# Kernel optimization log

Hardware: AMD Instinct MI355X
Metric: run time of the kernel (lower is better)

Reference implementation:

```python
import jax, jax.numpy as jnp
import numpy as np

N = 50000      # nodes
E = 800000     # edges (avg degree 16)
NE = 100000    # query edges
IN = 128; HID = 128; OUT = 128; FEAT = 2


def _linear_params(k, fan_in, fan_out):
    # torch.nn.Linear default init: U(-1/sqrt(fan_in), 1/sqrt(fan_in))
    s = 1.0 / np.sqrt(fan_in)
    k1, k2 = jax.random.split(k)
    W = jax.random.uniform(k1, (fan_in, fan_out), jnp.float32, -s, s)
    b = jax.random.uniform(k2, (fan_out,), jnp.float32, -s, s)
    return W, b


def setup_inputs() -> dict:
    key = jax.random.key(0)
    ks = jax.random.split(key, 9)
    inp = {}
    inp["x"] = jax.random.normal(ks[0], (N, IN), jnp.float32)
    inp["adj_t"] = jax.random.randint(ks[1], (2, E), 0, N)          # edge_index [2,E]
    inp["train_edges"] = jax.random.randint(ks[2], (NE, 2), 0, N)   # query edges
    # GCNConv stack params (lin weight + bias per layer)
    inp["W1"], inp["b1"] = _linear_params(ks[3], IN, HID)
    inp["W2"], inp["b2"] = _linear_params(ks[4], HID, HID)
    inp["W3"], inp["b3"] = _linear_params(ks[5], HID, OUT)
    # LinkPredictor MLP params
    inp["P1"], inp["pb1"] = _linear_params(ks[6], OUT, HID)
    inp["P2"], inp["pb2"] = _linear_params(ks[7], HID, HID)
    inp["P3"], inp["pb3"] = _linear_params(ks[8], HID, FEAT)
    return inp


def gcn_conv(x, edge_index, W, b):
    # GCNConv(normalize=False), edge_weight=None:
    #   h = x @ W; out[dst] += h[src]; out += bias
    h = x @ W                                    # [N, d_out]
    msg = h[edge_index[0]]                       # gather  [E, d_out]
    out = jax.ops.segment_sum(msg, edge_index[1], num_segments=x.shape[0])
    return out + b


def reference(x, adj_t, train_edges, W1, b1, W2, b2, W3, b3, P1, pb1, P2, pb2, P3, pb3):
    # GCN trunk (eval mode -> dropout is identity; dropout=0 anyway)
    h = jax.nn.relu(gcn_conv(x, adj_t, W1, b1))
    h = jax.nn.relu(gcn_conv(h, adj_t, W2, b2))
    emb = gcn_conv(h, adj_t, W3, b3)             # [N, OUT]
    # LinkPredictor on (src, dst) node-embedding pairs
    z = emb[train_edges[:, 0]] * emb[train_edges[:, 1]]   # [NE, OUT]
    z = jax.nn.relu(z @ P1 + pb1)
    z = jax.nn.relu(z @ P2 + pb2)
    z = z @ P3 + pb3                                       # [NE, FEAT]
    # F.normalize(p=2, dim=-1) with eps=1e-12
    z = z / jnp.maximum(jnp.linalg.norm(z, axis=-1, keepdims=True), 1e-12)
    pred = jax.nn.log_softmax(z, axis=-1)
    return pred[None]                                      # torch.unsqueeze(pred, 0)
```

## Files before the change

### kernel.cpp

```cpp
#include <hip/hip_runtime.h>
#include <math.h>

#define N_NODES 50000
#define N_EDGES 800000
#define N_QE    100000
#define D       128
#define NB      391
#define PCHUNK  8192

typedef _Float16 half8 __attribute__((ext_vector_type(8)));
typedef short    short8 __attribute__((ext_vector_type(8)));
typedef float    f32x4 __attribute__((ext_vector_type(4)));

static __device__ inline short f2bf(float f) {
    unsigned u = __builtin_bit_cast(unsigned, f);
    u += 0x7FFFu + ((u >> 16) & 1u);
    return (short)(u >> 16);
}

static const size_t O_CNT = 0;
static const size_t O_OFF = 256u * 1024;
static const size_t O_BC  = 512u * 1024;
static const size_t O_BS  = 768u * 1024;
static const size_t O_SRC = 1024u * 1024;
static const size_t O_TMP = 4u << 20;
static const size_t O_G   = 8u << 20;
static const size_t O_H   = O_G + 12800000u;
static const size_t O_T   = O_H + 12800000u;

__global__ void k_count(const int* __restrict__ dst, int* __restrict__ cnt) {
    int e = blockIdx.x * 256 + threadIdx.x;
    if (e < N_EDGES) atomicAdd(&cnt[dst[e]], 1);
}

__global__ __launch_bounds__(256)
void k_scan1(const int* __restrict__ cnt, int* __restrict__ off,
             int* __restrict__ bsum) {
    __shared__ int sh[256];
    const int t = threadIdx.x;
    const int i = blockIdx.x * 256 + t;
    int v = (i < N_NODES) ? cnt[i] : 0;
    sh[t] = v;
    __syncthreads();
    #pragma unroll
    for (int o = 1; o < 256; o <<= 1) {
        int u = (t >= o) ? sh[t - o] : 0;
        __syncthreads();
        sh[t] += u;
        __syncthreads();
    }
    if (i < N_NODES) off[i] = sh[t] - v;
    if (t == 255) bsum[blockIdx.x] = sh[255];
}

__global__ __launch_bounds__(256)
void k_scan2(int* __restrict__ bsum, int nblk) {
    __shared__ int sh[256];
    const int t = threadIdx.x;
    int v = (t < nblk) ? bsum[t] : 0;
    sh[t] = v;
    __syncthreads();
    #pragma unroll
    for (int o = 1; o < 256; o <<= 1) {
        int u = (t >= o) ? sh[t - o] : 0;
        __syncthreads();
        sh[t] += u;
        __syncthreads();
    }
    if (t < nblk) bsum[t] = sh[t] - v;
}

__global__ __launch_bounds__(256)
void k_scan3(int* __restrict__ off, const int* __restrict__ bsum) {
    const int i = blockIdx.x * 256 + threadIdx.x;
    if (i < N_NODES) off[i] = off[i] + bsum[blockIdx.x];
    if (i == 0) off[N_NODES] = N_EDGES;
}

__global__ void k_binit(const int* __restrict__ off, int* __restrict__ bcur) {
    int b = blockIdx.x * 256 + threadIdx.x;
    if (b < NB) bcur[b] = off[b << 7];
}

__global__ __launch_bounds__(256)
void k_part(const int* __restrict__ src, const int* __restrict__ dst,
            int* __restrict__ bcur, unsigned* __restrict__ tmp)
{
    __shared__ int hcnt[NB];
    __shared__ int lpos[NB];
    __shared__ int base[NB];
    const int t = threadIdx.x;
    const int e0 = blockIdx.x * PCHUNK;
    const int e1 = (e0 + PCHUNK < N_EDGES) ? e0 + PCHUNK : N_EDGES;

    for (int b = t; b < NB; b += 256) { hcnt[b] = 0; lpos[b] = 0; }
    __syncthreads();
    for (int e = e0 + t; e < e1; e += 256)
        atomicAdd(&hcnt[dst[e] >> 7], 1);
    __syncthreads();
    for (int b = t; b < NB; b += 256) {
        int c = hcnt[b];
        base[b] = c ? atomicAdd(&bcur[b], c) : 0;
    }
    __syncthreads();
    for (int e = e0 + t; e < e1; e += 256) {
        int d = dst[e];
        int b = d >> 7;
        int pos = atomicAdd(&lpos[b], 1);
        tmp[base[b] + pos] = (unsigned)src[e] | ((unsigned)(d & 127) << 16);
    }
}

__global__ __launch_bounds__(256)
void k_fine(const unsigned* __restrict__ tmp, const int* __restrict__ off,
            unsigned short* __restrict__ srcs)
{
    __shared__ int fcur[129];
    const int t = threadIdx.x;
    const int b = blockIdx.x;
    const int n0 = b << 7;
    const int nn = (N_NODES - n0 < 128) ? N_NODES - n0 : 128;
    if (t <= nn) fcur[t] = off[n0 + t];
    const int r0 = off[n0];
    const int r1 = off[n0 + nn];
    __syncthreads();
    for (int i = r0 + t; i < r1; i += 256) {
        unsigned en = tmp[i];
        int dl = en >> 16;
        int p = atomicAdd(&fcur[dl], 1);
        srcs[p] = (unsigned short)(en & 0xFFFFu);
    }
}

__global__ __launch_bounds__(256)
void k_t16all(const float* __restrict__ W1, const float* __restrict__ W2,
              const float* __restrict__ W3, const float* __restrict__ Q1,
              const float* __restrict__ Q2, short* __restrict__ T)
{
    int m = blockIdx.x >> 6;
    const float* S = (m == 0) ? W1 : (m == 1) ? W2 : (m == 2) ? W3
                   : (m == 3) ? Q1 : Q2;
    short* Dp = T + m * 16384;
    int idx = (blockIdx.x & 63) * 256 + threadIdx.x;
    int c = idx & 127, k = idx >> 7;
    Dp[c * 128 + k] = f2bf(S[k * 128 + c]);
}


template<typename XT>
__global__ __launch_bounds__(256)
void k_mm(const XT* __restrict__ X, const short* __restrict__ WT,
          _Float16* __restrict__ Y, int rows)
{
    __shared__ __align__(16) short xs[64 * 128];
    const int tid = threadIdx.x;
    const int l   = tid & 63;
    const int w   = tid >> 6;
    const int g   = l >> 4;
    const int l15 = l & 15;
    const int row0 = blockIdx.x * 64;

    {
        int r = tid >> 2;
        int gr = row0 + r; if (gr >= rows) gr = rows - 1;
        const XT* src = X + (size_t)gr * D;
        #pragma unroll
        for (int it = 0; it < 4; ++it) {
            int s = (tid & 3) + it * 4;
            short8 h;
            if constexpr (sizeof(XT) == 4) {
                float4 v0 = *(const float4*)((const float*)src + s * 8);
                float4 v1 = *(const float4*)((const float*)src + s * 8 + 4);
                h[0] = f2bf(v0.x); h[1] = f2bf(v0.y);
                h[2] = f2bf(v0.z); h[3] = f2bf(v0.w);
                h[4] = f2bf(v1.x); h[5] = f2bf(v1.y);
                h[6] = f2bf(v1.z); h[7] = f2bf(v1.w);
            } else {
                half8 v = *(const half8*)((const _Float16*)src + s * 8);
                #pragma unroll
                for (int c = 0; c < 8; ++c) h[c] = f2bf((float)v[c]);
            }
            *(short8*)&xs[r * 128 + ((s ^ (r & 7)) * 8)] = h;
        }
    }

    short8 wf[2][4];
    #pragma unroll
    for (int tt = 0; tt < 2; ++tt) {
        int c = w * 32 + tt * 16 + l15;
        #pragma unroll
        for (int s = 0; s < 4; ++s)
            wf[tt][s] = *(const short8*)(WT + (size_t)c * 128 + s * 32 + g * 8);
    }

    __syncthreads();

    f32x4 acc[4][2];
    #pragma unroll
    for (int rt = 0; rt < 4; ++rt)
        #pragma unroll
        for (int tt = 0; tt < 2; ++tt)
            acc[rt][tt] = (f32x4){0.f, 0.f, 0.f, 0.f};

    #pragma unroll
    for (int rt = 0; rt < 4; ++rt) {
        const int r = rt * 16 + l15;
        short8 a[4];
        #pragma unroll
        for (int s = 0; s < 4; ++s) {
            int slot = (4 * s + g) ^ (r & 7);
            a[s] = *(const short8*)&xs[r * 128 + slot * 8];
        }
        #pragma unroll
        for (int tt = 0; tt < 2; ++tt)
            #pragma unroll
            for (int s = 0; s < 4; ++s)
                acc[rt][tt] = __builtin_amdgcn_mfma_f32_16x16x32_bf16(
                    a[s], wf[tt][s], acc[rt][tt], 0, 0, 0);
    }

    __syncthreads();

    #pragma unroll
    for (int rt = 0; rt < 4; ++rt)
        #pragma unroll
        for (int tt = 0; tt < 2; ++tt) {
            int c = w * 32 + tt * 16 + l15;
            #pragma unroll
            for (int i = 0; i < 4; ++i) {
                int row = rt * 16 + g * 4 + i;
                int slot = (c >> 3) ^ (row & 7);
                xs[row * 128 + slot * 8 + (c & 7)] =
                    (short)__builtin_bit_cast(unsigned short, (_Float16)acc[rt][tt][i]);
            }
        }
    __syncthreads();

    {
        int r = tid >> 2;
        int gr = row0 + r;
        if (gr < rows) {
            short* dstp = (short*)(Y + (size_t)gr * D);
            #pragma unroll
            for (int it = 0; it < 4; ++it) {
                int s = (tid & 3) + it * 4;
                *(short8*)(dstp + s * 8) =
                    *(const short8*)&xs[r * 128 + ((s ^ (r & 7)) * 8)];
            }
        }
    }
}

template<bool RELU>
__global__ __launch_bounds__(256)
void k_agg(const _Float16* __restrict__ Hin, const int* __restrict__ off,
           const unsigned short* __restrict__ srcs, const float* __restrict__ bias,
           _Float16* __restrict__ Hout)
{
    const int lane = threadIdx.x & 63;
    const int es   = lane >> 4;
    const int q    = lane & 15;
    const int wv   = threadIdx.x >> 6;
    const int n    = blockIdx.x * 4 + wv;
    const int j0 = __builtin_amdgcn_readfirstlane(off[n]);
    const int j1 = __builtin_amdgcn_readfirstlane(off[n + 1]);

    float acc[8] = {};
    int j = j0;

    for (; j + 16 <= j1; j += 16) {
        half8 v[4];
        #pragma unroll
        for (int k = 0; k < 4; ++k) {
            int s = srcs[j + 4 * k + es];
            v[k] = *(const half8*)(Hin + (size_t)s * D + q * 8);
        }
        #pragma unroll
        for (int k = 0; k < 4; ++k)
            #pragma unroll
            for (int c = 0; c < 8; ++c) acc[c] += (float)v[k][c];
    }
    for (; j + 4 <= j1; j += 4) {
        int s = srcs[j + es];
        half8 v = *(const half8*)(Hin + (size_t)s * D + q * 8);
        #pragma unroll
        for (int c = 0; c < 8; ++c) acc[c] += (float)v[c];
    }
    {
        int rem = j1 - j;
        if (rem > 0) {
            int s = srcs[j + (es < rem ? es : rem - 1)];
            half8 v = *(const half8*)(Hin + (size_t)s * D + q * 8);
            if (es < rem) {
                #pragma unroll
                for (int c = 0; c < 8; ++c) acc[c] += (float)v[c];
            }
        }
    }

    #pragma unroll
    for (int c = 0; c < 8; ++c) {
        acc[c] += __shfl_xor(acc[c], 16, 64);
        acc[c] += __shfl_xor(acc[c], 32, 64);
    }

    if (es == 0) {
        half8 o;
        #pragma unroll
        for (int c = 0; c < 8; ++c) {
            float t = acc[c] + bias[q * 8 + c];
            if (RELU) t = fmaxf(t, 0.f);
            o[c] = (_Float16)t;
        }
        *(half8*)(Hout + (size_t)n * D + q * 8) = o;
    }
}

__global__ __launch_bounds__(256)
void k_predm(const _Float16* __restrict__ emb, const int* __restrict__ te,
             const short* __restrict__ P1T, const float* __restrict__ pb1,
             const short* __restrict__ P2T, const float* __restrict__ pb2,
             const float* __restrict__ P3, const float* __restrict__ pb3,
             float* __restrict__ out)
{
    __shared__ __align__(16) short xs[64 * 128];
    __shared__ float red[64][8];
    const int tid = threadIdx.x;
    const int l   = tid & 63;
    const int w   = tid >> 6;
    const int g   = l >> 4;
    const int l15 = l & 15;
    const int row0 = blockIdx.x * 64;

    {
        int r = tid >> 2;
        int e = row0 + r; if (e >= N_QE) e = N_QE - 1;
        const int2 ee = *(const int2*)(te + 2 * e);
        const _Float16* sp = emb + (size_t)ee.x * D;
        const _Float16* dp = emb + (size_t)ee.y * D;
        #pragma unroll
        for (int it = 0; it < 4; ++it) {
            int s = (tid & 3) + it * 4;
            half8 a = *(const half8*)(sp + s * 8);
            half8 b = *(const half8*)(dp + s * 8);
            short8 h;
            #pragma unroll
            for (int c = 0; c < 8; ++c) h[c] = f2bf((float)a[c] * (float)b[c]);
            *(short8*)&xs[r * 128 + ((s ^ (r & 7)) * 8)] = h;
        }
    }
    __syncthreads();

    f32x4 acc[4][2];

    {
        short8 wf[2][4];
        #pragma unroll
        for (int tt = 0; tt < 2; ++tt) {
            int c = w * 32 + tt * 16 + l15;
            #pragma unroll
            for (int s = 0; s < 4; ++s)
                wf[tt][s] = *(const short8*)(P1T + (size_t)c * 128 + s * 32 + g * 8);
        }
        #pragma unroll
        for (int rt = 0; rt < 4; ++rt)
            #pragma unroll
            for (int tt = 0; tt < 2; ++tt)
                acc[rt][tt] = (f32x4){0.f, 0.f, 0.f, 0.f};

        #pragma unroll
        for (int rt = 0; rt < 4; ++rt) {
            const int r = rt * 16 + l15;
            short8 a[4];
            #pragma unroll
            for (int s = 0; s < 4; ++s) {
                int slot = (4 * s + g) ^ (r & 7);
                a[s] = *(const short8*)&xs[r * 128 + slot * 8];
            }
            #pragma unroll
            for (int tt = 0; tt < 2; ++tt)
                #pragma unroll
                for (int s = 0; s < 4; ++s)
                    acc[rt][tt] = __builtin_amdgcn_mfma_f32_16x16x32_bf16(
                        a[s], wf[tt][s], acc[rt][tt], 0, 0, 0);
        }

        float bv[2];
        #pragma unroll
        for (int tt = 0; tt < 2; ++tt) bv[tt] = pb1[w * 32 + tt * 16 + l15];

        __syncthreads();

        #pragma unroll
        for (int rt = 0; rt < 4; ++rt)
            #pragma unroll
            for (int tt = 0; tt < 2; ++tt) {
                int c = w * 32 + tt * 16 + l15;
                #pragma unroll
                for (int i = 0; i < 4; ++i) {
                    float v = fmaxf(acc[rt][tt][i] + bv[tt], 0.f);
                    int row = rt * 16 + g * 4 + i;
                    int slot = (c >> 3) ^ (row & 7);
                    xs[row * 128 + slot * 8 + (c & 7)] = f2bf(v);
                }
            }
        __syncthreads();
    }

    {
        short8 wf[2][4];
        #pragma unroll
        for (int tt = 0; tt < 2; ++tt) {
            int c = w * 32 + tt * 16 + l15;
            #pragma unroll
            for (int s = 0; s < 4; ++s)
                wf[tt][s] = *(const short8*)(P2T + (size_t)c * 128 + s * 32 + g * 8);
        }
        #pragma unroll
        for (int rt = 0; rt < 4; ++rt)
            #pragma unroll
            for (int tt = 0; tt < 2; ++tt)
                acc[rt][tt] = (f32x4){0.f, 0.f, 0.f, 0.f};

        #pragma unroll
        for (int rt = 0; rt < 4; ++rt) {
            const int r = rt * 16 + l15;
            short8 a[4];
            #pragma unroll
            for (int s = 0; s < 4; ++s) {
                int slot = (4 * s + g) ^ (r & 7);
                a[s] = *(const short8*)&xs[r * 128 + slot * 8];
            }
            #pragma unroll
            for (int tt = 0; tt < 2; ++tt)
                #pragma unroll
                for (int s = 0; s < 4; ++s)
                    acc[rt][tt] = __builtin_amdgcn_mfma_f32_16x16x32_bf16(
                        a[s], wf[tt][s], acc[rt][tt], 0, 0, 0);
        }
    }

    {
        float bv[2];
        float2 p3v[2];
        #pragma unroll
        for (int tt = 0; tt < 2; ++tt) {
            int c = w * 32 + tt * 16 + l15;
            bv[tt] = pb2[c];
            p3v[tt] = *(const float2*)(P3 + c * 2);
        }
        #pragma unroll
        for (int rt = 0; rt < 4; ++rt)
            #pragma unroll
            for (int i = 0; i < 4; ++i) {
                float z0 = fmaxf(acc[rt][0][i] + bv[0], 0.f);
                float z1 = fmaxf(acc[rt][1][i] + bv[1], 0.f);
                float p0 = z0 * p3v[0].x + z1 * p3v[1].x;
                float p1 = z0 * p3v[0].y + z1 * p3v[1].y;
                #pragma unroll
                for (int o = 1; o < 16; o <<= 1) {
                    p0 += __shfl_xor(p0, o, 64);
                    p1 += __shfl_xor(p1, o, 64);
                }
                if (l15 == 0) {
                    int row = rt * 16 + g * 4 + i;
                    red[row][w * 2]     = p0;
                    red[row][w * 2 + 1] = p1;
                }
            }
    }
    __syncthreads();

    if (tid < 64) {
        int gr = row0 + tid;
        if (gr < N_QE) {
            float p0 = red[tid][0] + red[tid][2] + red[tid][4] + red[tid][6] + pb3[0];
            float p1 = red[tid][1] + red[tid][3] + red[tid][5] + red[tid][7] + pb3[1];
            float nrm = fmaxf(sqrtf(p0 * p0 + p1 * p1), 1e-12f);
            p0 /= nrm; p1 /= nrm;
            float m = fmaxf(p0, p1);
            float lse = m + logf(expf(p0 - m) + expf(p1 - m));
            out[gr * 2]     = p0 - lse;
            out[gr * 2 + 1] = p1 - lse;
        }
    }
}

extern "C" void kernel_launch(void* const* d_in, const int* in_sizes, int n_in,
                              void* d_out, int out_size, void* d_ws, size_t ws_size,
                              hipStream_t stream)
{
    (void)in_sizes; (void)n_in; (void)out_size; (void)ws_size;
    const float* x   = (const float*)d_in[0];
    const int*   adj = (const int*)d_in[1];
    const int*   te  = (const int*)d_in[2];
    const float* W1  = (const float*)d_in[3];
    const float* b1  = (const float*)d_in[4];
    const float* W2  = (const float*)d_in[5];
    const float* b2  = (const float*)d_in[6];
    const float* W3  = (const float*)d_in[7];
    const float* b3  = (const float*)d_in[8];
    const float* P1  = (const float*)d_in[9];
    const float* pb1 = (const float*)d_in[10];
    const float* P2  = (const float*)d_in[11];
    const float* pb2 = (const float*)d_in[12];
    const float* P3  = (const float*)d_in[13];
    const float* pb3 = (const float*)d_in[14];
    float* out = (float*)d_out;

    char* ws = (char*)d_ws;
    int* cnt  = (int*)(ws + O_CNT);
    int* off  = (int*)(ws + O_OFF);
    int* bcur = (int*)(ws + O_BC);
    int* bsum = (int*)(ws + O_BS);
    unsigned short* srcs = (unsigned short*)(ws + O_SRC);
    unsigned* tmp = (unsigned*)(ws + O_TMP);
    _Float16* G = (_Float16*)(ws + O_G);
    _Float16* H = (_Float16*)(ws + O_H);
    short*    T = (short*)(ws + O_T);

    const int* esrc = adj;
    const int* edst = adj + N_EDGES;

    const int SBLK = (N_NODES + 255) / 256;

    k_t16all<<<320, 256, 0, stream>>>(W1, W2, W3, P1, P2, T);

    hipMemsetAsync(cnt, 0, N_NODES * sizeof(int), stream);
    k_count<<<N_EDGES / 256, 256, 0, stream>>>(edst, cnt);
    k_scan1<<<SBLK, 256, 0, stream>>>(cnt, off, bsum);
    k_scan2<<<1, 256, 0, stream>>>(bsum, SBLK);
    k_scan3<<<SBLK, 256, 0, stream>>>(off, bsum);
    k_binit<<<2, 256, 0, stream>>>(off, bcur);
    k_part<<<(N_EDGES + PCHUNK - 1) / PCHUNK, 256, 0, stream>>>(esrc, edst, bcur, tmp);
    k_fine<<<NB, 256, 0, stream>>>(tmp, off, srcs);

    const int gN = (N_NODES + 63) / 64;

    k_mm<float><<<gN, 256, 0, stream>>>(x, T, H, N_NODES);
    k_agg<true><<<N_NODES / 4, 256, 0, stream>>>(H, off, srcs, b1, G);
    k_mm<_Float16><<<gN, 256, 0, stream>>>(G, T + 16384, H, N_NODES);
    k_agg<true><<<N_NODES / 4, 256, 0, stream>>>(H, off, srcs, b2, G);
    k_mm<_Float16><<<gN, 256, 0, stream>>>(G, T + 2 * 16384, H, N_NODES);
    k_agg<false><<<N_NODES / 4, 256, 0, stream>>>(H, off, srcs, b3, G);

    const int gQ = (N_QE + 63) / 64;
    k_predm<<<gQ, 256, 0, stream>>>(G, te, T + 3 * 16384, pb1,
                                    T + 4 * 16384, pb2, P3, pb3, out);
}
```

Measured before the change: 331.1 us.

## Split GCN aggregation into column quarters with 8 edges per wavefront step

The aggregation kernel now splits the 128 feature columns into four 32-column slices, each handled by its own grid partition. Within a slice, each wavefront processes 4 nodes, with 8 lanes per edge loading 4 halves each, so 8 edges are read in parallel. The idea is to keep a smaller working set of H columns hot in cache per pass and to use nontemporal stores for the output. In exchange, the neighbour index lists are re-read four times, loads narrow to 8 bytes, and the loop has no unrolling, which may reduce memory-level parallelism.

```diff
diff --git a/kernel.cpp b/kernel.cpp
--- a/kernel.cpp
+++ b/kernel.cpp
@@ -7,7 +7,9 @@
 #define D       128
 #define NB      391
 #define PCHUNK  8192
-
+#define NBLKQ   3125
+
+typedef _Float16 half4q __attribute__((ext_vector_type(4)));
 typedef _Float16 half8 __attribute__((ext_vector_type(8)));
 typedef short    short8 __attribute__((ext_vector_type(8)));
 typedef float    f32x4 __attribute__((ext_vector_type(4)));
@@ -257,62 +259,51 @@
            const unsigned short* __restrict__ srcs, const float* __restrict__ bias,
            _Float16* __restrict__ Hout)
 {
-    const int lane = threadIdx.x & 63;
-    const int es   = lane >> 4;
-    const int q    = lane & 15;
-    const int wv   = threadIdx.x >> 6;
-    const int n    = blockIdx.x * 4 + wv;
-    const int j0 = __builtin_amdgcn_readfirstlane(off[n]);
-    const int j1 = __builtin_amdgcn_readfirstlane(off[n + 1]);
-
-    float acc[8] = {};
-    int j = j0;
-
-    for (; j + 16 <= j1; j += 16) {
-        half8 v[4];
-        #pragma unroll
-        for (int k = 0; k < 4; ++k) {
-            int s = srcs[j + 4 * k + es];
-            v[k] = *(const half8*)(Hin + (size_t)s * D + q * 8);
-        }
-        #pragma unroll
-        for (int k = 0; k < 4; ++k)
-            #pragma unroll
-            for (int c = 0; c < 8; ++c) acc[c] += (float)v[k][c];
-    }
-    for (; j + 4 <= j1; j += 4) {
-        int s = srcs[j + es];
-        half8 v = *(const half8*)(Hin + (size_t)s * D + q * 8);
-        #pragma unroll
-        for (int c = 0; c < 8; ++c) acc[c] += (float)v[c];
-    }
-    {
-        int rem = j1 - j;
-        if (rem > 0) {
-            int s = srcs[j + (es < rem ? es : rem - 1)];
-            half8 v = *(const half8*)(Hin + (size_t)s * D + q * 8);
-            if (es < rem) {
-                #pragma unroll
-                for (int c = 0; c < 8; ++c) acc[c] += (float)v[c];
-            }
-        }
-    }
-
-    #pragma unroll
-    for (int c = 0; c < 8; ++c) {
-        acc[c] += __shfl_xor(acc[c], 16, 64);
-        acc[c] += __shfl_xor(acc[c], 32, 64);
-    }
-
-    if (es == 0) {
-        half8 o;
-        #pragma unroll
-        for (int c = 0; c < 8; ++c) {
-            float t = acc[c] + bias[q * 8 + c];
-            if (RELU) t = fmaxf(t, 0.f);
-            o[c] = (_Float16)t;
-        }
-        *(half8*)(Hout + (size_t)n * D + q * 8) = o;
+    const int l   = threadIdx.x & 63;
+    const int wv  = threadIdx.x >> 6;
+    const int es  = l >> 3;
+    const int qq  = l & 7;
+    const int p   = blockIdx.x / NBLKQ;
+    const int nb  = blockIdx.x % NBLKQ;
+    const int colbase = p * 32 + qq * 4;
+    const float4 bb = *(const float4*)(bias + colbase);
+
+    #pragma unroll
+    for (int i = 0; i < 4; ++i) {
+        const int n = nb * 16 + wv * 4 + i;
+        const int j0 = __builtin_amdgcn_readfirstlane(off[n]);
+        const int j1 = __builtin_amdgcn_readfirstlane(off[n + 1]);
+
+        float a0 = 0.f, a1 = 0.f, a2 = 0.f, a3 = 0.f;
+        for (int j = j0; j < j1; j += 8) {
+            if (es < j1 - j) {
+                int s = srcs[j + es];
+                half4q v = *(const half4q*)(Hin + (size_t)s * D + colbase);
+                a0 += (float)v[0]; a1 += (float)v[1];
+                a2 += (float)v[2]; a3 += (float)v[3];
+            }
+        }
+        #pragma unroll
+        for (int m = 8; m < 64; m <<= 1) {
+            a0 += __shfl_xor(a0, m, 64);
+            a1 += __shfl_xor(a1, m, 64);
+            a2 += __shfl_xor(a2, m, 64);
+            a3 += __shfl_xor(a3, m, 64);
+        }
+        if (es == 0) {
+            float t0 = a0 + bb.x, t1 = a1 + bb.y;
+            float t2 = a2 + bb.z, t3 = a3 + bb.w;
+            if (RELU) {
+                t0 = fmaxf(t0, 0.f); t1 = fmaxf(t1, 0.f);
+                t2 = fmaxf(t2, 0.f); t3 = fmaxf(t3, 0.f);
+            }
+            half4q o;
+            o[0] = (_Float16)t0; o[1] = (_Float16)t1;
+            o[2] = (_Float16)t2; o[3] = (_Float16)t3;
+            __builtin_nontemporal_store(
+                __builtin_bit_cast(unsigned long long, o),
+                (unsigned long long*)(Hout + (size_t)n * D + colbase));
+        }
     }
 }
 
@@ -538,11 +529,11 @@
     const int gN = (N_NODES + 63) / 64;
 
     k_mm<float><<<gN, 256, 0, stream>>>(x, T, H, N_NODES);
-    k_agg<true><<<N_NODES / 4, 256, 0, stream>>>(H, off, srcs, b1, G);
+    k_agg<true><<<4 * NBLKQ, 256, 0, stream>>>(H, off, srcs, b1, G);
     k_mm<_Float16><<<gN, 256, 0, stream>>>(G, T + 16384, H, N_NODES);
-    k_agg<true><<<N_NODES / 4, 256, 0, stream>>>(H, off, srcs, b2, G);
+    k_agg<true><<<4 * NBLKQ, 256, 0, stream>>>(H, off, srcs, b2, G);
     k_mm<_Float16><<<gN, 256, 0, stream>>>(G, T + 2 * 16384, H, N_NODES);
-    k_agg<false><<<N_NODES / 4, 256, 0, stream>>>(H, off, srcs, b3, G);
+    k_agg<false><<<4 * NBLKQ, 256, 0, stream>>>(H, off, srcs, b3, G);
 
     const int gQ = (N_QE + 63) / 64;
     k_predm<<<gQ, 256, 0, stream>>>(G, te, T + 3 * 16384, pb1,
```

Result: slower. 438.2 us (+32.4%).

## Build CSR via bucket-level counts and per-bucket local scans

Applied to the files above, without the earlier changes.

Replaces the per-node global atomic count and three-kernel scan with a per-chunk shared-memory histogram over 128-node buckets, a single-block bucket scan, and per-node offsets computed inside the fine partition kernel through a local count and scan. This removes 800k global atomics and several small kernel launches from CSR construction. In exchange the fine kernel reads its tmp slice twice, and the bucket scan assumes NB fits in 512 threads.

```diff
diff --git a/kernel.cpp b/kernel.cpp
--- a/kernel.cpp
+++ b/kernel.cpp
@@ -18,68 +18,49 @@
     return (short)(u >> 16);
 }
 
-static const size_t O_CNT = 0;
-static const size_t O_OFF = 256u * 1024;
-static const size_t O_BC  = 512u * 1024;
-static const size_t O_BS  = 768u * 1024;
-static const size_t O_SRC = 1024u * 1024;
-static const size_t O_TMP = 4u << 20;
-static const size_t O_G   = 8u << 20;
-static const size_t O_H   = O_G + 12800000u;
-static const size_t O_T   = O_H + 12800000u;
-
-__global__ void k_count(const int* __restrict__ dst, int* __restrict__ cnt) {
-    int e = blockIdx.x * 256 + threadIdx.x;
-    if (e < N_EDGES) atomicAdd(&cnt[dst[e]], 1);
-}
-
-__global__ __launch_bounds__(256)
-void k_scan1(const int* __restrict__ cnt, int* __restrict__ off,
-             int* __restrict__ bsum) {
-    __shared__ int sh[256];
+static const size_t O_BCNT = 0;
+static const size_t O_OFF  = 256u * 1024;
+static const size_t O_BC   = 512u * 1024;
+static const size_t O_BB   = 768u * 1024;
+static const size_t O_SRC  = 1024u * 1024;
+static const size_t O_TMP  = 4u << 20;
+static const size_t O_G    = 8u << 20;
+static const size_t O_H    = O_G + 12800000u;
+static const size_t O_T    = O_H + 12800000u;
+
+
+__global__ __launch_bounds__(256)
+void k_bcount(const int* __restrict__ dst, int* __restrict__ bcnt) {
+    __shared__ int h[NB];
     const int t = threadIdx.x;
-    const int i = blockIdx.x * 256 + t;
-    int v = (i < N_NODES) ? cnt[i] : 0;
+    const int e0 = blockIdx.x * PCHUNK;
+    const int e1 = (e0 + PCHUNK < N_EDGES) ? e0 + PCHUNK : N_EDGES;
+    for (int b = t; b < NB; b += 256) h[b] = 0;
+    __syncthreads();
+    for (int e = e0 + t; e < e1; e += 256)
+        atomicAdd(&h[dst[e] >> 7], 1);
+    __syncthreads();
+    for (int b = t; b < NB; b += 256)
+        if (h[b]) atomicAdd(&bcnt[b], h[b]);
+}
+
+__global__ __launch_bounds__(512)
+void k_bscan(const int* __restrict__ bcnt, int* __restrict__ bbase,
+             int* __restrict__ bcur, int* __restrict__ off) {
+    __shared__ int sh[512];
+    const int t = threadIdx.x;
+    int v = (t < NB) ? bcnt[t] : 0;
     sh[t] = v;
     __syncthreads();
     #pragma unroll
-    for (int o = 1; o < 256; o <<= 1) {
+    for (int o = 1; o < 512; o <<= 1) {
         int u = (t >= o) ? sh[t - o] : 0;
         __syncthreads();
         sh[t] += u;
         __syncthreads();
     }
-    if (i < N_NODES) off[i] = sh[t] - v;
-    if (t == 255) bsum[blockIdx.x] = sh[255];
-}
-
-__global__ __launch_bounds__(256)
-void k_scan2(int* __restrict__ bsum, int nblk) {
-    __shared__ int sh[256];
-    const int t = threadIdx.x;
-    int v = (t < nblk) ? bsum[t] : 0;
-    sh[t] = v;
-    __syncthreads();
-    #pragma unroll
-    for (int o = 1; o < 256; o <<= 1) {
-        int u = (t >= o) ? sh[t - o] : 0;
-        __syncthreads();
-        sh[t] += u;
-        __syncthreads();
-    }
-    if (t < nblk) bsum[t] = sh[t] - v;
-}
-
-__global__ __launch_bounds__(256)
-void k_scan3(int* __restrict__ off, const int* __restrict__ bsum) {
-    const int i = blockIdx.x * 256 + threadIdx.x;
-    if (i < N_NODES) off[i] = off[i] + bsum[blockIdx.x];
-    if (i == 0) off[N_NODES] = N_EDGES;
-}
-
-__global__ void k_binit(const int* __restrict__ off, int* __restrict__ bcur) {
-    int b = blockIdx.x * 256 + threadIdx.x;
-    if (b < NB) bcur[b] = off[b << 7];
+    if (t < NB) { int e = sh[t] - v; bbase[t] = e; bcur[t] = e; }
+    if (t == 0) { bbase[NB] = N_EDGES; off[N_NODES] = N_EDGES; }
 }
 
 __global__ __launch_bounds__(256)
@@ -112,22 +93,40 @@
 }
 
 __global__ __launch_bounds__(256)
-void k_fine(const unsigned* __restrict__ tmp, const int* __restrict__ off,
-            unsigned short* __restrict__ srcs)
-{
-    __shared__ int fcur[129];
+void k_fine2(const unsigned* __restrict__ tmp, const int* __restrict__ bbase,
+             unsigned short* __restrict__ srcs, int* __restrict__ off)
+{
+    __shared__ int ncnt[128];
+    __shared__ int fcur[128];
     const int t = threadIdx.x;
     const int b = blockIdx.x;
     const int n0 = b << 7;
     const int nn = (N_NODES - n0 < 128) ? N_NODES - n0 : 128;
-    if (t <= nn) fcur[t] = off[n0 + t];
-    const int r0 = off[n0];
-    const int r1 = off[n0 + nn];
+    const int r0 = bbase[b];
+    const int r1 = bbase[b + 1];
+
+    if (t < 128) ncnt[t] = 0;
+    __syncthreads();
+    for (int i = r0 + t; i < r1; i += 256)
+        atomicAdd(&ncnt[tmp[i] >> 16], 1);
+    __syncthreads();
+    int c = (t < 128) ? ncnt[t] : 0;
+    #pragma unroll
+    for (int o = 1; o < 128; o <<= 1) {
+        int u = (t >= o && t < 128) ? ncnt[t - o] : 0;
+        __syncthreads();
+        if (t < 128) ncnt[t] += u;
+        __syncthreads();
+    }
+    if (t < 128) {
+        int excl = r0 + ncnt[t] - c;
+        fcur[t] = excl;
+        if (t < nn) off[n0 + t] = excl;
+    }
     __syncthreads();
     for (int i = r0 + t; i < r1; i += 256) {
         unsigned en = tmp[i];
-        int dl = en >> 16;
-        int p = atomicAdd(&fcur[dl], 1);
+        int p = atomicAdd(&fcur[en >> 16], 1);
         srcs[p] = (unsigned short)(en & 0xFFFFu);
     }
 }
@@ -509,10 +508,10 @@
     float* out = (float*)d_out;
 
     char* ws = (char*)d_ws;
-    int* cnt  = (int*)(ws + O_CNT);
+    int* bcnt = (int*)(ws + O_BCNT);
     int* off  = (int*)(ws + O_OFF);
     int* bcur = (int*)(ws + O_BC);
-    int* bsum = (int*)(ws + O_BS);
+    int* bbase= (int*)(ws + O_BB);
     unsigned short* srcs = (unsigned short*)(ws + O_SRC);
     unsigned* tmp = (unsigned*)(ws + O_TMP);
     _Float16* G = (_Float16*)(ws + O_G);
@@ -521,19 +520,15 @@
 
     const int* esrc = adj;
     const int* edst = adj + N_EDGES;
-
-    const int SBLK = (N_NODES + 255) / 256;
+    const int NCHUNK = (N_EDGES + PCHUNK - 1) / PCHUNK;
 
     k_t16all<<<320, 256, 0, stream>>>(W1, W2, W3, P1, P2, T);
 
-    hipMemsetAsync(cnt, 0, N_NODES * sizeof(int), stream);
-    k_count<<<N_EDGES / 256, 256, 0, stream>>>(edst, cnt);
-    k_scan1<<<SBLK, 256, 0, stream>>>(cnt, off, bsum);
-    k_scan2<<<1, 256, 0, stream>>>(bsum, SBLK);
-    k_scan3<<<SBLK, 256, 0, stream>>>(off, bsum);
-    k_binit<<<2, 256, 0, stream>>>(off, bcur);
-    k_part<<<(N_EDGES + PCHUNK - 1) / PCHUNK, 256, 0, stream>>>(esrc, edst, bcur, tmp);
-    k_fine<<<NB, 256, 0, stream>>>(tmp, off, srcs);
+    hipMemsetAsync(bcnt, 0, NB * sizeof(int), stream);
+    k_bcount<<<NCHUNK, 256, 0, stream>>>(edst, bcnt);
+    k_bscan<<<1, 512, 0, stream>>>(bcnt, bbase, bcur, off);
+    k_part<<<NCHUNK, 256, 0, stream>>>(esrc, edst, bcur, tmp);
+    k_fine2<<<NB, 256, 0, stream>>>(tmp, bbase, srcs, off);
 
     const int gN = (N_NODES + 63) / 64;
 
```

New measurement: 298.6 us (median of 2 runs). -9.8%, faster.
